# Performance work log

Measured on AMD Instinct MI355X. Metric: run time of the kernel, lower is better.

## Reference

```python
import jax, jax.numpy as jnp
import numpy as np

B, S, D = 1, 4096, 512
INNER = 512
K, PAD = 3, 1
MAX_OUT = 4 * S  # static padded output length (torch uses data-dependent max)
EPS = 1e-5
TINY_SLOWDOWN = 0.5


def _conv1d(x, w, b):
    # x: [B, C_in, S], w: [C_out, C_in, K] -> [B, C_out, S]
    y = jax.lax.conv_general_dilated(x, w, window_strides=(1,), padding=[(PAD, PAD)],
                                     dimension_numbers=('NCH', 'OIH', 'NCH'))
    return y + b[None, :, None]


def _layernorm(x, g, b):
    m = jnp.mean(x, axis=-1, keepdims=True)
    v = jnp.var(x, axis=-1, keepdims=True)
    return (x - m) * jax.lax.rsqrt(v + EPS) * g + b


def _duration_predictor(enc, c1w, c1b, g1, b1, c2w, c2b, g2, b2, lw, lb):
    # enc: [B, S, D]; dropout is identity (eval mode)
    x = _conv1d(enc.transpose(0, 2, 1), c1w, c1b).transpose(0, 2, 1)   # [B,S,INNER]
    x = jax.nn.relu(_layernorm(x, g1, b1))
    x = _conv1d(x.transpose(0, 2, 1), c2w, c2b).transpose(0, 2, 1)     # [B,S,INNER]
    x = jax.nn.relu(_layernorm(x, g2, b2))
    out = jax.nn.relu(jnp.einsum('bsd,od->bso', x, lw) + lb)           # [B,S,1]
    return out[..., 0]                                                  # [B,S] (B==1 => matches squeeze/unsqueeze(0))


def setup_inputs() -> dict:
    key = jax.random.key(0)
    ks = jax.random.split(key, 4)
    return {
        'enc_output': jax.random.normal(ks[0], (B, S, D), dtype=jnp.float32),
        'conv1_w': jax.random.normal(ks[1], (INNER, D, K), dtype=jnp.float32) * 0.02,
        'conv1_b': jnp.zeros((INNER,), jnp.float32),
        'ln1_g': jnp.ones((INNER,), jnp.float32),
        'ln1_b': jnp.zeros((INNER,), jnp.float32),
        'conv2_w': jax.random.normal(ks[2], (INNER, INNER, K), dtype=jnp.float32) * 0.02,
        'conv2_b': jnp.zeros((INNER,), jnp.float32),
        'ln2_g': jnp.ones((INNER,), jnp.float32),
        'ln2_b': jnp.zeros((INNER,), jnp.float32),
        'lin_w': jax.random.normal(ks[3], (1, INNER), jnp.float32) * 0.1,
        'lin_b': jnp.zeros((1,), jnp.float32),
    }


def reference(enc_output, conv1_w, conv1_b, ln1_g, ln1_b, conv2_w, conv2_b,
              ln2_g, ln2_b, lin_w, lin_b):
    pred = _duration_predictor(enc_output, conv1_w, conv1_b, ln1_g, ln1_b,
                               conv2_w, conv2_b, ln2_g, ln2_b, lin_w, lin_b)
    dur = jnp.floor(pred + TINY_SLOWDOWN).astype(jnp.int32)            # [B,S], nonneg so floor == int()
    cum = jnp.cumsum(dur, axis=-1)                                     # [B,S]
    t = jnp.arange(MAX_OUT, dtype=jnp.int32)                           # [T]
    # frame t belongs to phoneme i where cum[i-1] <= t < cum[i]
    idx = jax.vmap(lambda c: jnp.searchsorted(c, t, side='right'))(cum)  # [B,T]
    valid = t[None, :] < cum[:, -1:]                                   # [B,T]
    idx = jnp.clip(idx, 0, S - 1)
    gathered = jnp.take_along_axis(enc_output, idx[:, :, None], axis=1)  # [B,T,D]
    mod_enc_output = jnp.where(valid[:, :, None], gathered, jnp.zeros((), enc_output.dtype))
    output_pos = jnp.arange(1, MAX_OUT + 1, dtype=jnp.int64 if jax.config.jax_enable_x64 else jnp.int32)[None, :]
    return mod_enc_output, output_pos
```

## Files before the change

kernel.cpp:

```cpp
#include <hip/hip_runtime.h>

#define S      4096
#define D      512
#define KWIN   3
#define SP     (S + 2)
#define MAXOUT 16384
#define EPSLN  1e-5f
#define NIT    16
#define NKT    48

typedef __attribute__((ext_vector_type(8))) short short8;
typedef __attribute__((ext_vector_type(4))) float floatx4;

__device__ inline ushort f2bf(float x) {
  union { float f; unsigned u; } v; v.f = x;
  unsigned r = v.u + 0x7fffu + ((v.u >> 16) & 1u);
  return (ushort)(r >> 16);
}
__device__ inline float bf2f(ushort h) {
  union { float f; unsigned u; } v; v.u = ((unsigned)h) << 16;
  return v.f;
}

__global__ __launch_bounds__(256) void pack_x_kernel(const float* __restrict__ x,
                                                     ushort* __restrict__ ph,
                                                     ushort* __restrict__ pl) {
  int t = blockIdx.x * 256 + threadIdx.x;
  if (t >= SP * D) return;
  int g = t >> 9;
  int i = t & 511;
  float v = (g == 0 || g == SP - 1) ? 0.0f : x[(size_t)(g - 1) * D + i];
  ushort hi = f2bf(v);
  ushort lo = f2bf(v - bf2f(hi));
  size_t dst = ((size_t)(i >> 5) * SP + g) * 32 + (i & 31);
  ph[dst] = hi;
  pl[dst] = lo;
}

__global__ __launch_bounds__(256) void t1pad_kernel(ushort* __restrict__ th,
                                                    ushort* __restrict__ tl) {
  for (int idx = threadIdx.x; idx < NIT * 2 * 32; idx += 256) {
    int c   = idx >> 6;
    int rr  = (idx >> 5) & 1;
    int col = idx & 31;
    size_t off = ((size_t)c * SP + (rr ? (SP - 1) : 0)) * 32 + col;
    th[off] = 0;
    tl[off] = 0;
  }
}

__global__ __launch_bounds__(256) void wtrans_pack_kernel(const float* __restrict__ w,
                                                          ushort* __restrict__ bh,
                                                          ushort* __restrict__ bl) {
  int t = blockIdx.x * 256 + threadIdx.x;
  if (t >= D * D * KWIN) return;
  float v = w[t];
  int o   = t / (D * KWIN);
  int rem = t - o * (D * KWIN);
  int i   = rem / KWIN;
  int k   = rem - i * KWIN;
  ushort hi = f2bf(v);
  ushort lo = f2bf(v - bf2f(hi));
  size_t dst = ((size_t)(k * NIT + (i >> 5)) * D + o) * 32 + (i & 31);
  bh[dst] = hi;
  bl[dst] = lo;
}

__device__ inline void gload16(const void* g, void* l) {
  __builtin_amdgcn_global_load_lds((const __attribute__((address_space(1))) void*)g,
                                   (__attribute__((address_space(3))) void*)l,
                                   16, 0, 0);
}

__global__ __launch_bounds__(256) void gemm_mfma_kernel(
    const ushort* __restrict__ Ah, const ushort* __restrict__ Al,
    const ushort* __restrict__ Bh, const ushort* __restrict__ Bl,
    float* __restrict__ C) {
  __shared__ __align__(16) ushort Ahs[64 * 32];
  __shared__ __align__(16) ushort Als[64 * 32];
  __shared__ __align__(16) ushort Bhs[64 * 32];
  __shared__ __align__(16) ushort Bls[64 * 32];

  const int tid  = threadIdx.x;
  const int wave = tid >> 6;
  const int lane = tid & 63;
  const int row0 = blockIdx.x * 64;
  const int col0 = blockIdx.y * 64;
  const int wm0  = (wave >> 1) * 32;
  const int wn0  = (wave & 1) * 32;
  const int fr   = lane & 15;
  const int quad = lane >> 4;

  floatx4 acc[2][2] = {};

  ushort* sbase = (wave == 0) ? Ahs : (wave == 1) ? Als : (wave == 2) ? Bhs : Bls;

  for (int kt = 0; kt < NKT; ++kt) {
    const int tap   = kt >> 4;
    const int itile = kt & 15;
    const ushort* gb;
    if (wave == 0)      gb = Ah + ((size_t)itile * SP + row0 + tap) * 32;
    else if (wave == 1) gb = Al + ((size_t)itile * SP + row0 + tap) * 32;
    else if (wave == 2) gb = Bh + ((size_t)kt * D + col0) * 32;
    else                gb = Bl + ((size_t)kt * D + col0) * 32;

    __syncthreads();
#pragma unroll
    for (int seg = 0; seg < 4; ++seg)
      gload16(gb + seg * 512 + lane * 8, sbase + seg * 512);
    asm volatile("s_waitcnt vmcnt(0)" ::: "memory");
    __syncthreads();

    short8 ah[2], al2[2], bh[2], bl2[2];
#pragma unroll
    for (int mf = 0; mf < 2; ++mf) {
      ah[mf]  = *(const short8*)&Ahs[(wm0 + mf * 16 + fr) * 32 + quad * 8];
      al2[mf] = *(const short8*)&Als[(wm0 + mf * 16 + fr) * 32 + quad * 8];
    }
#pragma unroll
    for (int nf = 0; nf < 2; ++nf) {
      bh[nf]  = *(const short8*)&Bhs[(wn0 + nf * 16 + fr) * 32 + quad * 8];
      bl2[nf] = *(const short8*)&Bls[(wn0 + nf * 16 + fr) * 32 + quad * 8];
    }
#pragma unroll
    for (int mf = 0; mf < 2; ++mf)
#pragma unroll
      for (int nf = 0; nf < 2; ++nf) {
        acc[mf][nf] = __builtin_amdgcn_mfma_f32_16x16x32_bf16(ah[mf],  bh[nf],  acc[mf][nf], 0, 0, 0);
        acc[mf][nf] = __builtin_amdgcn_mfma_f32_16x16x32_bf16(ah[mf],  bl2[nf], acc[mf][nf], 0, 0, 0);
        acc[mf][nf] = __builtin_amdgcn_mfma_f32_16x16x32_bf16(al2[mf], bh[nf],  acc[mf][nf], 0, 0, 0);
      }
  }

#pragma unroll
  for (int mf = 0; mf < 2; ++mf)
#pragma unroll
    for (int nf = 0; nf < 2; ++nf) {
      const int col = col0 + wn0 + nf * 16 + fr;
#pragma unroll
      for (int r = 0; r < 4; ++r) {
        const int row = row0 + wm0 + mf * 16 + quad * 4 + r;
        C[(size_t)row * D + col] = acc[mf][nf][r];
      }
    }
}

__global__ __launch_bounds__(256) void ln_relu_pack_kernel(
    const float* __restrict__ X, const float* __restrict__ cb,
    const float* __restrict__ gam, const float* __restrict__ bet,
    ushort* __restrict__ th, ushort* __restrict__ tl) {
  const int wave = threadIdx.x >> 6;
  const int lane = threadIdx.x & 63;
  const int s = blockIdx.x * 4 + wave;
  const float4* xp = (const float4*)(X + (size_t)s * D);
  float4 a = xp[2 * lane];
  float4 b = xp[2 * lane + 1];
  const float4 ca  = ((const float4*)cb)[2 * lane];
  const float4 cb2 = ((const float4*)cb)[2 * lane + 1];
  float v[8] = {a.x + ca.x,  a.y + ca.y,  a.z + ca.z,  a.w + ca.w,
                b.x + cb2.x, b.y + cb2.y, b.z + cb2.z, b.w + cb2.w};
  float sum = 0.f;
#pragma unroll
  for (int i = 0; i < 8; ++i) sum += v[i];
#pragma unroll
  for (int off = 32; off > 0; off >>= 1) sum += __shfl_xor(sum, off);
  const float m = sum * (1.0f / D);
  float sq = 0.f;
#pragma unroll
  for (int i = 0; i < 8; ++i) { v[i] -= m; sq += v[i] * v[i]; }
#pragma unroll
  for (int off = 32; off > 0; off >>= 1) sq += __shfl_xor(sq, off);
  const float rs = rsqrtf(sq * (1.0f / D) + EPSLN);
  const float4 ga = ((const float4*)gam)[2 * lane];
  const float4 gb = ((const float4*)gam)[2 * lane + 1];
  const float4 ba = ((const float4*)bet)[2 * lane];
  const float4 bb = ((const float4*)bet)[2 * lane + 1];
  const float gg[8] = {ga.x, ga.y, ga.z, ga.w, gb.x, gb.y, gb.z, gb.w};
  const float bt[8] = {ba.x, ba.y, ba.z, ba.w, bb.x, bb.y, bb.z, bb.w};
  short8 h8, l8;
#pragma unroll
  for (int i = 0; i < 8; ++i) {
    float y = fmaxf(v[i] * rs * gg[i] + bt[i], 0.0f);
    ushort hi = f2bf(y);
    h8[i] = (short)hi;
    l8[i] = (short)f2bf(y - bf2f(hi));
  }
  const size_t base = ((size_t)(lane >> 2) * SP + (s + 1)) * 32 + (size_t)(lane & 3) * 8;
  *(short8*)(th + base) = h8;
  *(short8*)(tl + base) = l8;
}

__global__ __launch_bounds__(256) void ln2_pred_kernel(
    const float* __restrict__ X, const float* __restrict__ cb,
    const float* __restrict__ gam, const float* __restrict__ bet,
    const float* __restrict__ lw, const float* __restrict__ lb,
    int* __restrict__ dur) {
  const int wave = threadIdx.x >> 6;
  const int lane = threadIdx.x & 63;
  const int s = blockIdx.x * 4 + wave;
  const float4* xp = (const float4*)(X + (size_t)s * D);
  float4 a = xp[2 * lane];
  float4 b = xp[2 * lane + 1];
  const float4 ca  = ((const float4*)cb)[2 * lane];
  const float4 cb2 = ((const float4*)cb)[2 * lane + 1];
  float v[8] = {a.x + ca.x,  a.y + ca.y,  a.z + ca.z,  a.w + ca.w,
                b.x + cb2.x, b.y + cb2.y, b.z + cb2.z, b.w + cb2.w};
  float sum = 0.f;
#pragma unroll
  for (int i = 0; i < 8; ++i) sum += v[i];
#pragma unroll
  for (int off = 32; off > 0; off >>= 1) sum += __shfl_xor(sum, off);
  const float m = sum * (1.0f / D);
  float sq = 0.f;
#pragma unroll
  for (int i = 0; i < 8; ++i) { v[i] -= m; sq += v[i] * v[i]; }
#pragma unroll
  for (int off = 32; off > 0; off >>= 1) sq += __shfl_xor(sq, off);
  const float rs = rsqrtf(sq * (1.0f / D) + EPSLN);
  const float4 ga = ((const float4*)gam)[2 * lane];
  const float4 gb = ((const float4*)gam)[2 * lane + 1];
  const float4 ba = ((const float4*)bet)[2 * lane];
  const float4 bb = ((const float4*)bet)[2 * lane + 1];
  const float gg[8] = {ga.x, ga.y, ga.z, ga.w, gb.x, gb.y, gb.z, gb.w};
  const float bt[8] = {ba.x, ba.y, ba.z, ba.w, bb.x, bb.y, bb.z, bb.w};
  const float4 w0 = ((const float4*)lw)[2 * lane];
  const float4 w1 = ((const float4*)lw)[2 * lane + 1];
  const float ww[8] = {w0.x, w0.y, w0.z, w0.w, w1.x, w1.y, w1.z, w1.w};
  float d = 0.f;
#pragma unroll
  for (int i = 0; i < 8; ++i) {
    float y = fmaxf(v[i] * rs * gg[i] + bt[i], 0.0f);
    d += y * ww[i];
  }
#pragma unroll
  for (int off = 32; off > 0; off >>= 1) d += __shfl_xor(d, off);
  if (lane == 0) {
    const float p = fmaxf(d + lb[0], 0.0f);
    dur[s] = (int)floorf(p + 0.5f);
  }
}

__global__ __launch_bounds__(1024) void scan_kernel(const int* __restrict__ dur,
                                                    int* __restrict__ cum) {
  __shared__ int sd[1024];
  const int tid = threadIdx.x;
  const int4 d = *(const int4*)(dur + (tid << 2));
  const int l0 = d.x;
  const int l1 = l0 + d.y;
  const int l2 = l1 + d.z;
  const int l3 = l2 + d.w;
  sd[tid] = l3;
  __syncthreads();
  for (int off = 1; off < 1024; off <<= 1) {
    int v = 0;
    if (tid >= off) v = sd[tid - off];
    __syncthreads();
    sd[tid] += v;
    __syncthreads();
  }
  const int base = (tid > 0) ? sd[tid - 1] : 0;
  int4 o;
  o.x = base + l0; o.y = base + l1; o.z = base + l2; o.w = base + l3;
  *(int4*)(cum + (tid << 2)) = o;
}

__global__ __launch_bounds__(256) void gather_kernel(
    const float* __restrict__ enc, const int* __restrict__ cum,
    float* __restrict__ out0, float* __restrict__ out1) {
  const int half = threadIdx.x >> 7;
  const int d4   = (threadIdx.x & 127) << 2;
  const int t    = blockIdx.x * 2 + half;
  const int total = cum[S - 1];

  int lo = 0, hi = S;
  while (lo < hi) {
    const int mid = (lo + hi) >> 1;
    if (cum[mid] <= t) lo = mid + 1; else hi = mid;
  }
  const int idx = (lo < S) ? lo : (S - 1);

  float4 v = make_float4(0.f, 0.f, 0.f, 0.f);
  if (t < total) v = *(const float4*)(enc + (size_t)idx * D + d4);
  *(float4*)(out0 + (size_t)t * D + d4) = v;

  if ((threadIdx.x & 127) == 0) out1[t] = (float)(t + 1);
}

extern "C" void kernel_launch(void* const* d_in, const int* in_sizes, int n_in,
                              void* d_out, int out_size, void* d_ws, size_t ws_size,
                              hipStream_t stream) {
  const float* enc = (const float*)d_in[0];
  const float* w1  = (const float*)d_in[1];
  const float* cb1 = (const float*)d_in[2];
  const float* g1  = (const float*)d_in[3];
  const float* be1 = (const float*)d_in[4];
  const float* w2  = (const float*)d_in[5];
  const float* cb2 = (const float*)d_in[6];
  const float* g2  = (const float*)d_in[7];
  const float* be2 = (const float*)d_in[8];
  const float* lw  = (const float*)d_in[9];
  const float* lb  = (const float*)d_in[10];

  float* out0 = (float*)d_out;
  float* out1 = out0 + (size_t)MAXOUT * D;

  const size_t NP = (size_t)NIT * SP * 32;
  const size_t NB = (size_t)NKT * D * 32;
  ushort* Xph = (ushort*)d_ws;
  ushort* Xpl = Xph + NP;
  ushort* T1h = Xpl + NP;
  ushort* T1l = T1h + NP;
  ushort* Bph = T1l + NP;
  ushort* Bpl = Bph + NB;
  float*  t0  = (float*)(Bpl + NB);
  int*   dur  = (int*)(t0 + (size_t)S * D);
  int*   cum  = dur + S;

  pack_x_kernel<<<(SP * D + 255) / 256, 256, 0, stream>>>(enc, Xph, Xpl);
  t1pad_kernel<<<1, 256, 0, stream>>>(T1h, T1l);
  wtrans_pack_kernel<<<(D * D * KWIN + 255) / 256, 256, 0, stream>>>(w1, Bph, Bpl);
  gemm_mfma_kernel<<<dim3(S / 64, D / 64), 256, 0, stream>>>(Xph, Xpl, Bph, Bpl, t0);
  ln_relu_pack_kernel<<<S / 4, 256, 0, stream>>>(t0, cb1, g1, be1, T1h, T1l);
  wtrans_pack_kernel<<<(D * D * KWIN + 255) / 256, 256, 0, stream>>>(w2, Bph, Bpl);
  gemm_mfma_kernel<<<dim3(S / 64, D / 64), 256, 0, stream>>>(T1h, T1l, Bph, Bpl, t0);
  ln2_pred_kernel<<<S / 4, 256, 0, stream>>>(t0, cb2, g2, be2, lw, lb, dur);
  scan_kernel<<<1, 1024, 0, stream>>>(dur, cum);
  gather_kernel<<<MAXOUT / 2, 256, 0, stream>>>(enc, cum, out0, out1);
}
```

Measured before the change: 203.1 us.

## Double-buffer GEMM K-loop, merge pack kernels, and use single-wave scan

The GEMM now stages two K-tiles per step into a double-buffered LDS array and prefetches the next pair while computing the current one. This removes the explicit vmcnt wait and halves the barrier count. The x, w1, w2 and pad-zeroing pack kernels are merged into one launch. The weight pack is reindexed so its writes are coalesced, and both weight packs get their own buffers so w2 packing no longer sits between the GEMMs. The 1024-thread shared-memory scan is replaced by a single-wave register scan using shuffles, at the cost of more LDS per GEMM block and a larger workspace.

Result: faster. 165.1 us (-18.7%).

```diff
diff --git a/kernel.cpp b/kernel.cpp
--- a/kernel.cpp
+++ b/kernel.cpp
@@ -8,6 +8,7 @@
 #define EPSLN  1e-5f
 #define NIT    16
 #define NKT    48
+#define NPAIR  24
 
 typedef __attribute__((ext_vector_type(8))) short short8;
 typedef __attribute__((ext_vector_type(4))) float floatx4;
@@ -22,48 +23,51 @@
   return v.f;
 }
 
-__global__ __launch_bounds__(256) void pack_x_kernel(const float* __restrict__ x,
-                                                     ushort* __restrict__ ph,
-                                                     ushort* __restrict__ pl) {
-  int t = blockIdx.x * 256 + threadIdx.x;
-  if (t >= SP * D) return;
-  int g = t >> 9;
-  int i = t & 511;
-  float v = (g == 0 || g == SP - 1) ? 0.0f : x[(size_t)(g - 1) * D + i];
-  ushort hi = f2bf(v);
-  ushort lo = f2bf(v - bf2f(hi));
-  size_t dst = ((size_t)(i >> 5) * SP + g) * 32 + (i & 31);
-  ph[dst] = hi;
-  pl[dst] = lo;
-}
-
-__global__ __launch_bounds__(256) void t1pad_kernel(ushort* __restrict__ th,
-                                                    ushort* __restrict__ tl) {
-  for (int idx = threadIdx.x; idx < NIT * 2 * 32; idx += 256) {
-    int c   = idx >> 6;
-    int rr  = (idx >> 5) & 1;
-    int col = idx & 31;
-    size_t off = ((size_t)c * SP + (rr ? (SP - 1) : 0)) * 32 + col;
-    th[off] = 0;
-    tl[off] = 0;
-  }
-}
-
-__global__ __launch_bounds__(256) void wtrans_pack_kernel(const float* __restrict__ w,
-                                                          ushort* __restrict__ bh,
-                                                          ushort* __restrict__ bl) {
-  int t = blockIdx.x * 256 + threadIdx.x;
-  if (t >= D * D * KWIN) return;
-  float v = w[t];
-  int o   = t / (D * KWIN);
-  int rem = t - o * (D * KWIN);
-  int i   = rem / KWIN;
-  int k   = rem - i * KWIN;
-  ushort hi = f2bf(v);
-  ushort lo = f2bf(v - bf2f(hi));
-  size_t dst = ((size_t)(k * NIT + (i >> 5)) * D + o) * 32 + (i & 31);
-  bh[dst] = hi;
-  bl[dst] = lo;
+#define NB0 8196
+#define NB1 3072
+#define NB3 4
+
+__device__ inline void wpack(const float* __restrict__ w, ushort* __restrict__ bh,
+                             ushort* __restrict__ bl, int idx) {
+  const int kk = idx & 31;
+  const int o  = (idx >> 5) & 511;
+  const int it = (idx >> 14) & 15;
+  const int k  = idx >> 18;
+  const float v = w[o * (D * KWIN) + (it * 32 + kk) * KWIN + k];
+  const ushort hi = f2bf(v);
+  bh[idx] = hi;
+  bl[idx] = f2bf(v - bf2f(hi));
+}
+
+__global__ __launch_bounds__(256) void pack_all_kernel(
+    const float* __restrict__ x, const float* __restrict__ w1,
+    const float* __restrict__ w2, ushort* __restrict__ Xph,
+    ushort* __restrict__ Xpl, ushort* __restrict__ B1h, ushort* __restrict__ B1l,
+    ushort* __restrict__ B2h, ushort* __restrict__ B2l,
+    ushort* __restrict__ T1h, ushort* __restrict__ T1l) {
+  const int b = blockIdx.x;
+  if (b < NB0) {
+    const int t = b * 256 + threadIdx.x;
+    const int g = t >> 9;
+    const int i = t & 511;
+    const float v = (g == 0 || g == SP - 1) ? 0.0f : x[(size_t)(g - 1) * D + i];
+    const ushort hi = f2bf(v);
+    const size_t dst = ((size_t)(i >> 5) * SP + g) * 32 + (i & 31);
+    Xph[dst] = hi;
+    Xpl[dst] = f2bf(v - bf2f(hi));
+  } else if (b < NB0 + NB1) {
+    wpack(w1, B1h, B1l, (b - NB0) * 256 + threadIdx.x);
+  } else if (b < NB0 + 2 * NB1) {
+    wpack(w2, B2h, B2l, (b - NB0 - NB1) * 256 + threadIdx.x);
+  } else {
+    const int idx = (b - NB0 - 2 * NB1) * 256 + threadIdx.x;
+    const int c   = idx >> 6;
+    const int rr  = (idx >> 5) & 1;
+    const int col = idx & 31;
+    const size_t off = ((size_t)c * SP + (rr ? (SP - 1) : 0)) * 32 + col;
+    T1h[off] = 0;
+    T1l[off] = 0;
+  }
 }
 
 __device__ inline void gload16(const void* g, void* l) {
@@ -76,10 +80,7 @@
     const ushort* __restrict__ Ah, const ushort* __restrict__ Al,
     const ushort* __restrict__ Bh, const ushort* __restrict__ Bl,
     float* __restrict__ C) {
-  __shared__ __align__(16) ushort Ahs[64 * 32];
-  __shared__ __align__(16) ushort Als[64 * 32];
-  __shared__ __align__(16) ushort Bhs[64 * 32];
-  __shared__ __align__(16) ushort Bls[64 * 32];
+  __shared__ __align__(16) ushort smem[2][4][2][2048];
 
   const int tid  = threadIdx.x;
   const int wave = tid >> 6;
@@ -93,43 +94,60 @@
 
   floatx4 acc[2][2] = {};
 
-  ushort* sbase = (wave == 0) ? Ahs : (wave == 1) ? Als : (wave == 2) ? Bhs : Bls;
-
-  for (int kt = 0; kt < NKT; ++kt) {
+  auto gbase = [&](int kt) -> const ushort* {
     const int tap   = kt >> 4;
     const int itile = kt & 15;
-    const ushort* gb;
-    if (wave == 0)      gb = Ah + ((size_t)itile * SP + row0 + tap) * 32;
-    else if (wave == 1) gb = Al + ((size_t)itile * SP + row0 + tap) * 32;
-    else if (wave == 2) gb = Bh + ((size_t)kt * D + col0) * 32;
-    else                gb = Bl + ((size_t)kt * D + col0) * 32;
-
+    if (wave == 0)      return Ah + ((size_t)itile * SP + row0 + tap) * 32;
+    else if (wave == 1) return Al + ((size_t)itile * SP + row0 + tap) * 32;
+    else if (wave == 2) return Bh + ((size_t)kt * D + col0) * 32;
+    else                return Bl + ((size_t)kt * D + col0) * 32;
+  };
+
+  auto stage = [&](int p, int db) {
+    ushort* ldsb = &smem[db][wave][0][0];
+#pragma unroll
+    for (int sub = 0; sub < 2; ++sub) {
+      const ushort* gb = gbase(2 * p + sub);
+#pragma unroll
+      for (int seg = 0; seg < 4; ++seg)
+        gload16(gb + seg * 512 + lane * 8, ldsb + sub * 2048 + seg * 512);
+    }
+  };
+
+  stage(0, 0);
+
+  for (int p = 0; p < NPAIR; ++p) {
+    const int db = p & 1;
     __syncthreads();
-#pragma unroll
-    for (int seg = 0; seg < 4; ++seg)
-      gload16(gb + seg * 512 + lane * 8, sbase + seg * 512);
-    asm volatile("s_waitcnt vmcnt(0)" ::: "memory");
-    __syncthreads();
-
-    short8 ah[2], al2[2], bh[2], bl2[2];
-#pragma unroll
-    for (int mf = 0; mf < 2; ++mf) {
-      ah[mf]  = *(const short8*)&Ahs[(wm0 + mf * 16 + fr) * 32 + quad * 8];
-      al2[mf] = *(const short8*)&Als[(wm0 + mf * 16 + fr) * 32 + quad * 8];
+    if (p + 1 < NPAIR) stage(p + 1, db ^ 1);
+
+    const ushort* As_h = &smem[db][0][0][0];
+    const ushort* As_l = &smem[db][1][0][0];
+    const ushort* Bs_h = &smem[db][2][0][0];
+    const ushort* Bs_l = &smem[db][3][0][0];
+#pragma unroll
+    for (int sub = 0; sub < 2; ++sub) {
+      const int so = sub * 2048;
+      short8 ah[2], al2[2], bh[2], bl2[2];
+#pragma unroll
+      for (int mf = 0; mf < 2; ++mf) {
+        ah[mf]  = *(const short8*)&As_h[so + (wm0 + mf * 16 + fr) * 32 + quad * 8];
+        al2[mf] = *(const short8*)&As_l[so + (wm0 + mf * 16 + fr) * 32 + quad * 8];
+      }
+#pragma unroll
+      for (int nf = 0; nf < 2; ++nf) {
+        bh[nf]  = *(const short8*)&Bs_h[so + (wn0 + nf * 16 + fr) * 32 + quad * 8];
+        bl2[nf] = *(const short8*)&Bs_l[so + (wn0 + nf * 16 + fr) * 32 + quad * 8];
+      }
+#pragma unroll
+      for (int mf = 0; mf < 2; ++mf)
+#pragma unroll
+        for (int nf = 0; nf < 2; ++nf) {
+          acc[mf][nf] = __builtin_amdgcn_mfma_f32_16x16x32_bf16(ah[mf],  bh[nf],  acc[mf][nf], 0, 0, 0);
+          acc[mf][nf] = __builtin_amdgcn_mfma_f32_16x16x32_bf16(ah[mf],  bl2[nf], acc[mf][nf], 0, 0, 0);
+          acc[mf][nf] = __builtin_amdgcn_mfma_f32_16x16x32_bf16(al2[mf], bh[nf],  acc[mf][nf], 0, 0, 0);
+        }
     }
-#pragma unroll
-    for (int nf = 0; nf < 2; ++nf) {
-      bh[nf]  = *(const short8*)&Bhs[(wn0 + nf * 16 + fr) * 32 + quad * 8];
-      bl2[nf] = *(const short8*)&Bls[(wn0 + nf * 16 + fr) * 32 + quad * 8];
-    }
-#pragma unroll
-    for (int mf = 0; mf < 2; ++mf)
-#pragma unroll
-      for (int nf = 0; nf < 2; ++nf) {
-        acc[mf][nf] = __builtin_amdgcn_mfma_f32_16x16x32_bf16(ah[mf],  bh[nf],  acc[mf][nf], 0, 0, 0);
-        acc[mf][nf] = __builtin_amdgcn_mfma_f32_16x16x32_bf16(ah[mf],  bl2[nf], acc[mf][nf], 0, 0, 0);
-        acc[mf][nf] = __builtin_amdgcn_mfma_f32_16x16x32_bf16(al2[mf], bh[nf],  acc[mf][nf], 0, 0, 0);
-      }
   }
 
 #pragma unroll
@@ -240,28 +258,33 @@
   }
 }
 
-__global__ __launch_bounds__(1024) void scan_kernel(const int* __restrict__ dur,
-                                                    int* __restrict__ cum) {
-  __shared__ int sd[1024];
-  const int tid = threadIdx.x;
-  const int4 d = *(const int4*)(dur + (tid << 2));
-  const int l0 = d.x;
-  const int l1 = l0 + d.y;
-  const int l2 = l1 + d.z;
-  const int l3 = l2 + d.w;
-  sd[tid] = l3;
-  __syncthreads();
-  for (int off = 1; off < 1024; off <<= 1) {
-    int v = 0;
-    if (tid >= off) v = sd[tid - off];
-    __syncthreads();
-    sd[tid] += v;
-    __syncthreads();
-  }
-  const int base = (tid > 0) ? sd[tid - 1] : 0;
-  int4 o;
-  o.x = base + l0; o.y = base + l1; o.z = base + l2; o.w = base + l3;
-  *(int4*)(cum + (tid << 2)) = o;
+__global__ __launch_bounds__(64) void scan_kernel(const int* __restrict__ dur,
+                                                  int* __restrict__ cum) {
+  const int lane = threadIdx.x;
+  const int4* src = (const int4*)dur + (size_t)lane * 16;
+  int4 v[16];
+  int run = 0;
+#pragma unroll
+  for (int i = 0; i < 16; ++i) {
+    int4 d = src[i];
+    d.x += run; d.y += d.x; d.z += d.y; d.w += d.z;
+    run = d.w;
+    v[i] = d;
+  }
+  int sc = run;
+#pragma unroll
+  for (int off = 1; off < 64; off <<= 1) {
+    const int n = __shfl_up(sc, off);
+    if (lane >= off) sc += n;
+  }
+  const int base = sc - run;
+  int4* dst = (int4*)cum + (size_t)lane * 16;
+#pragma unroll
+  for (int i = 0; i < 16; ++i) {
+    int4 d = v[i];
+    d.x += base; d.y += base; d.z += base; d.w += base;
+    dst[i] = d;
+  }
 }
 
 __global__ __launch_bounds__(256) void gather_kernel(
@@ -310,20 +333,20 @@
   ushort* Xpl = Xph + NP;
   ushort* T1h = Xpl + NP;
   ushort* T1l = T1h + NP;
-  ushort* Bph = T1l + NP;
-  ushort* Bpl = Bph + NB;
-  float*  t0  = (float*)(Bpl + NB);
+  ushort* B1h = T1l + NP;
+  ushort* B1l = B1h + NB;
+  ushort* B2h = B1l + NB;
+  ushort* B2l = B2h + NB;
+  float*  t0  = (float*)(B2l + NB);
   int*   dur  = (int*)(t0 + (size_t)S * D);
   int*   cum  = dur + S;
 
-  pack_x_kernel<<<(SP * D + 255) / 256, 256, 0, stream>>>(enc, Xph, Xpl);
-  t1pad_kernel<<<1, 256, 0, stream>>>(T1h, T1l);
-  wtrans_pack_kernel<<<(D * D * KWIN + 255) / 256, 256, 0, stream>>>(w1, Bph, Bpl);
-  gemm_mfma_kernel<<<dim3(S / 64, D / 64), 256, 0, stream>>>(Xph, Xpl, Bph, Bpl, t0);
+  pack_all_kernel<<<NB0 + 2 * NB1 + NB3, 256, 0, stream>>>(
+      enc, w1, w2, Xph, Xpl, B1h, B1l, B2h, B2l, T1h, T1l);
+  gemm_mfma_kernel<<<dim3(S / 64, D / 64), 256, 0, stream>>>(Xph, Xpl, B1h, B1l, t0);
   ln_relu_pack_kernel<<<S / 4, 256, 0, stream>>>(t0, cb1, g1, be1, T1h, T1l);
-  wtrans_pack_kernel<<<(D * D * KWIN + 255) / 256, 256, 0, stream>>>(w2, Bph, Bpl);
-  gemm_mfma_kernel<<<dim3(S / 64, D / 64), 256, 0, stream>>>(T1h, T1l, Bph, Bpl, t0);
+  gemm_mfma_kernel<<<dim3(S / 64, D / 64), 256, 0, stream>>>(T1h, T1l, B2h, B2l, t0);
   ln2_pred_kernel<<<S / 4, 256, 0, stream>>>(t0, cb2, g2, be2, lw, lb, dur);
-  scan_kernel<<<1, 1024, 0, stream>>>(dur, cum);
+  scan_kernel<<<1, 64, 0, stream>>>(dur, cum);
   gather_kernel<<<MAXOUT / 2, 256, 0, stream>>>(enc, cum, out0, out1);
 }
```
